# Performance work log

Hardware: AMD Instinct MI355X
Metric: run time of the kernel (lower is better)

Reference implementation:

```python
import jax, jax.numpy as jnp
import numpy as np
import math

B, CIN, COUT, K, SD, H, W = 16, 512, 512, 3, 512, 32, 32


def setup_inputs() -> dict:
    key = jax.random.key(0)
    ks = jax.random.split(key, 7)
    return {
        "x": jax.random.normal(ks[0], (B, CIN, H, W), jnp.float32),
        "style": jax.random.normal(ks[1], (B, SD), jnp.float32),
        "noise": jax.random.normal(ks[2], (B, 1, H, W), jnp.float32),
        "weight": jax.random.normal(ks[3], (COUT, CIN, K, K), jnp.float32),
        "mod_w": jax.random.normal(ks[4], (CIN, SD), jnp.float32),
        "mod_b": jnp.ones((CIN,), jnp.float32),
        "noise_weight": jax.random.normal(ks[5], (1,), jnp.float32) * 0.1,
        "act_bias": jax.random.normal(ks[6], (COUT,), jnp.float32) * 0.1,
    }


def reference(x, style, noise, weight, mod_w, mod_b, noise_weight, act_bias):
    conv_scale = 1.0 / math.sqrt(CIN * K * K)  # equalized-lr scale of ModulatedConv2d
    mod_scale = 1.0 / math.sqrt(SD)            # EqualLinear scale (lr_mul=1)

    # style modulation: EqualLinear(style_dim -> in_channel), bias init 1
    s = style @ (mod_w.T * mod_scale) + mod_b              # [B, CIN]

    # per-sample modulated weights [B, COUT, CIN, K, K]
    w = conv_scale * weight[None] * s[:, None, :, None, None]

    # demodulation
    demod = jax.lax.rsqrt(jnp.sum(w * w, axis=(2, 3, 4)) + 1e-8)  # [B, COUT]
    w = w * demod[:, :, None, None, None]

    # grouped (per-sample) conv: vmap a single-sample conv over the batch
    pad = K // 2

    def conv1(xi, wi):
        return jax.lax.conv_general_dilated(
            xi[None], wi, window_strides=(1, 1),
            padding=[(pad, pad), (pad, pad)],
            dimension_numbers=("NCHW", "OIHW", "NCHW"))[0]

    out = jax.vmap(conv1)(x, w)  # [B, COUT, H, W]

    # NoiseInjection: out + weight * noise (scalar learned weight)
    out = out + noise_weight[0] * noise

    # FusedLeakyReLU: leaky_relu(out + bias, 0.2) * sqrt(2)
    out = jax.nn.leaky_relu(out + act_bias[None, :, None, None], 0.2) * math.sqrt(2.0)
    return out
```

## Files before the change

### kernel.cpp

```cpp
#include <hip/hip_runtime.h>
#include <cstdint>
#include <cstddef>

typedef unsigned short u16;
typedef __attribute__((ext_vector_type(8))) short short8;
typedef __attribute__((ext_vector_type(4))) float f32x4;

#define CIN   512
#define COUT  512
#define BATCH 16
#define HWSZ  1024
#define PADW  34

static constexpr float MOD_SCALE  = 0.044194173824159216f;
static constexpr float CONV_SCALE = 0.014731391274719739f;

#define WS_S    0
#define WS_DSC  (32*1024)
#define WS_WSQ  (64*1024)
#define WS_WBT  (64*1024 + 1024*1024)
#define WS_XSP  (WS_WBT + 9*512*512*2)

__device__ __forceinline__ u16 f2bf(float f) {
  union { float f; uint32_t u; } v; v.f = f;
  uint32_t r = v.u + 0x7fffu + ((v.u >> 16) & 1u);
  return (u16)(r >> 16);
}

__device__ __forceinline__ void gload16(const void* g, void* l) {
  __builtin_amdgcn_global_load_lds(
      (const __attribute__((address_space(1))) void*)g,
      (__attribute__((address_space(3))) void*)l, 16, 0, 0);
}

__global__ void k_style(const float* __restrict__ style, const float* __restrict__ mod_w,
                        const float* __restrict__ mod_b, float* __restrict__ s_out) {
  int gid  = blockIdx.x * blockDim.x + threadIdx.x;
  int w    = gid >> 6, lane = gid & 63;
  int b    = w >> 9, i = w & 511;
  const float4* st = (const float4*)(style + (size_t)b * 512);
  const float4* mw = (const float4*)(mod_w + (size_t)i * 512);
  float4 a0 = st[lane * 2], a1 = st[lane * 2 + 1];
  float4 w0 = mw[lane * 2], w1 = mw[lane * 2 + 1];
  float acc = a0.x*w0.x + a0.y*w0.y + a0.z*w0.z + a0.w*w0.w
            + a1.x*w1.x + a1.y*w1.y + a1.z*w1.z + a1.w*w1.w;
  #pragma unroll
  for (int off = 32; off; off >>= 1) acc += __shfl_xor(acc, off);
  if (lane == 0) s_out[w] = acc * MOD_SCALE + mod_b[i];
}

__global__ void k_wprep(const float* __restrict__ w, float* __restrict__ wsq,
                        u16* __restrict__ wbt) {
  int idx = blockIdx.x * 256 + threadIdx.x;
  const float* p = w + (size_t)idx * 9;
  float a = 0.f;
  #pragma unroll
  for (int kxy = 0; kxy < 9; ++kxy) {
    float v = p[kxy];
    a += v * v;
    wbt[(size_t)kxy * 262144 + idx] = f2bf(v);
  }
  wsq[idx] = a;
}

__global__ void k_dscale(const float* __restrict__ wsq, const float* __restrict__ s,
                         float* __restrict__ dsc) {
  int gid  = blockIdx.x * blockDim.x + threadIdx.x;
  int w    = gid >> 6, lane = gid & 63;
  int b    = w >> 9, o = w & 511;
  const float4* q4 = (const float4*)(wsq + (size_t)o * 512);
  const float4* s4 = (const float4*)(s   + (size_t)b * 512);
  float4 q0 = q4[lane * 2], q1 = q4[lane * 2 + 1];
  float4 t0 = s4[lane * 2], t1 = s4[lane * 2 + 1];
  float acc = q0.x*t0.x*t0.x + q0.y*t0.y*t0.y + q0.z*t0.z*t0.z + q0.w*t0.w*t0.w
            + q1.x*t1.x*t1.x + q1.y*t1.y*t1.y + q1.z*t1.z*t1.z + q1.w*t1.w*t1.w;
  #pragma unroll
  for (int off = 32; off; off >>= 1) acc += __shfl_xor(acc, off);
  if (lane == 0)
    dsc[w] = CONV_SCALE * rsqrtf(acc * CONV_SCALE * CONV_SCALE + 1e-8f);
}

__global__ void k_xs(const float* __restrict__ x, const float* __restrict__ s,
                     u16* __restrict__ xsp) {
  __shared__ float tile[64][33];
  int icb = blockIdx.x, y = blockIdx.y, b = blockIdx.z;
  int t = threadIdx.x;
  int i0 = icb * 64;
  int c  = t & 31;
  int r0 = t >> 5;
  #pragma unroll
  for (int it = 0; it < 8; ++it) {
    int row = r0 + it * 8;
    float sv = s[b * 512 + i0 + row];
    tile[row][c] = x[((size_t)(b * 512 + i0 + row)) * 1024 + y * 32 + c] * sv;
  }
  __syncthreads();
  int il = t & 63;
  int x0 = t >> 6;
  #pragma unroll
  for (int it = 0; it < 8; ++it) {
    int xc = x0 + it * 4;
    xsp[((size_t)((b * PADW + y + 1) * PADW) + (xc + 1)) * 512 + i0 + il] = f2bf(tile[il][xc]);
  }
}

__global__ __launch_bounds__(256) void k_conv(
    const u16* __restrict__ wbt, const u16* __restrict__ xsp,
    const float* __restrict__ dsc, const float* __restrict__ noise,
    const float* __restrict__ nw, const float* __restrict__ abias,
    float* __restrict__ out)
{
  __shared__ u16 Ald[128 * 64];
  __shared__ u16 Bld[128 * 64];

  const int tid  = threadIdx.x;
  const int wave = tid >> 6, lane = tid & 63;
  const int o0 = blockIdx.x * 128;
  const int m0 = blockIdx.y * 128;
  const int b  = m0 >> 10;

  const u16* gA[4]; const u16* gB[4]; u16* lA[4]; u16* lB[4];
  const int cc = (((lane & 7) ^ (lane >> 3)) * 8);
  #pragma unroll
  for (int q = 0; q < 4; ++q) {
    int r  = wave * 32 + q * 8 + (lane >> 3);
    gA[q] = wbt + (size_t)(o0 + r) * 512 + cc;
    int mg = m0 + r;
    int yy = (mg >> 5) & 31, xx = mg & 31;
    gB[q] = xsp + ((size_t)(b * PADW + yy) * PADW + xx) * 512 + cc;
    lA[q] = &Ald[(wave * 32 + q * 8) * 64];
    lB[q] = &Bld[(wave * 32 + q * 8) * 64];
  }

  f32x4 acc[4][4];
  #pragma unroll
  for (int i = 0; i < 4; ++i)
    #pragma unroll
    for (int j = 0; j < 4; ++j) acc[i][j] = (f32x4){0.f, 0.f, 0.f, 0.f};

  const int wo = (wave >> 1) * 64;
  const int wm = (wave & 1) * 64;
  const int lrow = lane & 15;
  const int lk   = (lane >> 4) * 8;
  const int rsw  = (lrow & 7) << 3;

  for (int ks = 0; ks < 72; ++ks) {
    int kxy = ks >> 3;
    int ib  = (ks & 7) << 6;
    int ky  = kxy / 3, kx = kxy - ky * 3;
    int offA = kxy * 262144 + ib;
    int offB = ((ky * PADW + kx) << 9) + ib;

    __syncthreads();
    #pragma unroll
    for (int q = 0; q < 4; ++q) gload16(gA[q] + offA, lA[q]);
    #pragma unroll
    for (int q = 0; q < 4; ++q) gload16(gB[q] + offB, lB[q]);
    asm volatile("s_waitcnt vmcnt(0)" ::: "memory");
    __syncthreads();

    #pragma unroll
    for (int kh = 0; kh < 2; ++kh) {
      int kos = (kh * 32 + lk) ^ rsw;
      short8 av[4], bv[4];
      #pragma unroll
      for (int mi = 0; mi < 4; ++mi)
        av[mi] = *(const short8*)&Ald[(wo + mi * 16 + lrow) * 64 + kos];
      #pragma unroll
      for (int ni = 0; ni < 4; ++ni)
        bv[ni] = *(const short8*)&Bld[(wm + ni * 16 + lrow) * 64 + kos];
      #pragma unroll
      for (int mi = 0; mi < 4; ++mi)
        #pragma unroll
        for (int ni = 0; ni < 4; ++ni)
          acc[mi][ni] = __builtin_amdgcn_mfma_f32_16x16x32_bf16(
              av[mi], bv[ni], acc[mi][ni], 0, 0, 0);
    }
  }

  const float nwv = nw[0];
  const int mrow = (lane >> 4) << 2;
  #pragma unroll
  for (int mi = 0; mi < 4; ++mi) {
    #pragma unroll
    for (int ni = 0; ni < 4; ++ni) {
      int mg = m0 + wm + ni * 16 + lrow;
      int hw = mg & 1023;
      float nz = nwv * noise[b * 1024 + hw];
      #pragma unroll
      for (int r = 0; r < 4; ++r) {
        int og = o0 + wo + mi * 16 + mrow + r;
        float v = acc[mi][ni][r] * dsc[b * 512 + og] + nz + abias[og];
        v = (v > 0.f ? v : 0.2f * v) * 1.4142135623730951f;
        out[(size_t)(b * 512 + og) * 1024 + hw] = v;
      }
    }
  }
}

extern "C" void kernel_launch(void* const* d_in, const int* in_sizes, int n_in,
                              void* d_out, int out_size, void* d_ws, size_t ws_size,
                              hipStream_t stream) {
  const float* x      = (const float*)d_in[0];
  const float* style  = (const float*)d_in[1];
  const float* noise  = (const float*)d_in[2];
  const float* weight = (const float*)d_in[3];
  const float* mod_w  = (const float*)d_in[4];
  const float* mod_b  = (const float*)d_in[5];
  const float* nw     = (const float*)d_in[6];
  const float* abias  = (const float*)d_in[7];
  float* out = (float*)d_out;

  char* ws = (char*)d_ws;
  float* s_buf = (float*)(ws + WS_S);
  float* dsc   = (float*)(ws + WS_DSC);
  float* wsq   = (float*)(ws + WS_WSQ);
  u16*   wbt   = (u16*)(ws + WS_WBT);
  u16*   xsp   = (u16*)(ws + WS_XSP);

  hipMemsetAsync(xsp, 0, (size_t)BATCH * PADW * PADW * 512 * 2, stream);

  k_style <<<2048, 256, 0, stream>>>(style, mod_w, mod_b, s_buf);
  k_wprep <<<1024, 256, 0, stream>>>(weight, wsq, wbt);
  k_dscale<<<2048, 256, 0, stream>>>(wsq, s_buf, dsc);
  k_xs    <<<dim3(8, 32, 16), 256, 0, stream>>>(x, s_buf, xsp);
  k_conv  <<<dim3(4, 128), 256, 0, stream>>>(wbt, xsp, dsc, noise, nw, abias, out);
}
```

Before: 126.6 us.

## Triple-buffer conv GEMM loads with larger 256x128 tiles and block swizzle

Rewrites the main loop of the implicit-GEMM conv as a three-stage LDS ring. Asynchronous global-to-LDS loads for later K-steps are issued before computing the current one, and partial vmcnt waits replace the full drain before each barrier. Blocks grow to 512 threads, each computing a 256x128 output tile, and a linear grid with a swizzled block index replaces the 2D grid. This hides global load latency behind MFMA work and lets the larger tile reuse each loaded activation more. The cost is about 144KB of LDS per block, which limits each CU to one resident block, and fewer blocks overall.

```diff
diff --git a/kernel.cpp b/kernel.cpp
--- a/kernel.cpp
+++ b/kernel.cpp
@@ -104,32 +104,40 @@
   }
 }
 
-__global__ __launch_bounds__(256) void k_conv(
+__global__ __launch_bounds__(512, 2) void k_conv(
     const u16* __restrict__ wbt, const u16* __restrict__ xsp,
     const float* __restrict__ dsc, const float* __restrict__ noise,
     const float* __restrict__ nw, const float* __restrict__ abias,
     float* __restrict__ out)
 {
-  __shared__ u16 Ald[128 * 64];
-  __shared__ u16 Bld[128 * 64];
+  __shared__ u16 Ald[3 * 16384];
+  __shared__ u16 Bld[3 * 8192];
 
   const int tid  = threadIdx.x;
   const int wave = tid >> 6, lane = tid & 63;
-  const int o0 = blockIdx.x * 128;
-  const int m0 = blockIdx.y * 128;
+
+  const int bid = blockIdx.x;
+  const int swz = (bid & 7) * 32 + (bid >> 3);
+  const int o0 = (swz >> 7) << 8;
+  const int m0 = (swz & 127) << 7;
   const int b  = m0 >> 10;
 
-  const u16* gA[4]; const u16* gB[4]; u16* lA[4]; u16* lB[4];
   const int cc = (((lane & 7) ^ (lane >> 3)) * 8);
+  const u16* gA[4]; int lAo[4];
   #pragma unroll
   for (int q = 0; q < 4; ++q) {
-    int r  = wave * 32 + q * 8 + (lane >> 3);
+    int r = wave * 32 + q * 8 + (lane >> 3);
     gA[q] = wbt + (size_t)(o0 + r) * 512 + cc;
+    lAo[q] = (wave * 32 + q * 8) * 64;
+  }
+  const u16* gB[2]; int lBo[2];
+  #pragma unroll
+  for (int q = 0; q < 2; ++q) {
+    int r = wave * 16 + q * 8 + (lane >> 3);
     int mg = m0 + r;
     int yy = (mg >> 5) & 31, xx = mg & 31;
     gB[q] = xsp + ((size_t)(b * PADW + yy) * PADW + xx) * 512 + cc;
-    lA[q] = &Ald[(wave * 32 + q * 8) * 64];
-    lB[q] = &Bld[(wave * 32 + q * 8) * 64];
+    lBo[q] = (wave * 16 + q * 8) * 64;
   }
 
   f32x4 acc[4][4];
@@ -144,31 +152,28 @@
   const int lk   = (lane >> 4) * 8;
   const int rsw  = (lrow & 7) << 3;
 
-  for (int ks = 0; ks < 72; ++ks) {
-    int kxy = ks >> 3;
-    int ib  = (ks & 7) << 6;
-    int ky  = kxy / 3, kx = kxy - ky * 3;
+  auto stage = [&](int ks, int sa, int sb) {
+    int kxy = ks >> 3, ib = (ks & 7) << 6;
+    int ky = kxy / 3, kx = kxy - ky * 3;
     int offA = kxy * 262144 + ib;
     int offB = ((ky * PADW + kx) << 9) + ib;
-
-    __syncthreads();
-    #pragma unroll
-    for (int q = 0; q < 4; ++q) gload16(gA[q] + offA, lA[q]);
-    #pragma unroll
-    for (int q = 0; q < 4; ++q) gload16(gB[q] + offB, lB[q]);
-    asm volatile("s_waitcnt vmcnt(0)" ::: "memory");
-    __syncthreads();
-
+    #pragma unroll
+    for (int q = 0; q < 4; ++q) gload16(gA[q] + offA, &Ald[sa + lAo[q]]);
+    #pragma unroll
+    for (int q = 0; q < 2; ++q) gload16(gB[q] + offB, &Bld[sb + lBo[q]]);
+  };
+
+  auto compute = [&](int ca, int cb) {
     #pragma unroll
     for (int kh = 0; kh < 2; ++kh) {
       int kos = (kh * 32 + lk) ^ rsw;
       short8 av[4], bv[4];
       #pragma unroll
       for (int mi = 0; mi < 4; ++mi)
-        av[mi] = *(const short8*)&Ald[(wo + mi * 16 + lrow) * 64 + kos];
+        av[mi] = *(const short8*)&Ald[ca + (wo + mi * 16 + lrow) * 64 + kos];
       #pragma unroll
       for (int ni = 0; ni < 4; ++ni)
-        bv[ni] = *(const short8*)&Bld[(wm + ni * 16 + lrow) * 64 + kos];
+        bv[ni] = *(const short8*)&Bld[cb + (wm + ni * 16 + lrow) * 64 + kos];
       #pragma unroll
       for (int mi = 0; mi < 4; ++mi)
         #pragma unroll
@@ -176,6 +181,26 @@
           acc[mi][ni] = __builtin_amdgcn_mfma_f32_16x16x32_bf16(
               av[mi], bv[ni], acc[mi][ni], 0, 0, 0);
     }
+  };
+
+  stage(0, 0, 0);
+  stage(1, 16384, 8192);
+
+  for (int t = 0; t < 24; ++t) {
+    int k0 = t * 3;
+    asm volatile("s_waitcnt vmcnt(6)" ::: "memory");
+    __builtin_amdgcn_s_barrier();
+    if (k0 + 2 < 72) stage(k0 + 2, 32768, 16384);
+    compute(0, 0);
+    asm volatile("s_waitcnt vmcnt(6)" ::: "memory");
+    __builtin_amdgcn_s_barrier();
+    if (k0 + 3 < 72) stage(k0 + 3, 0, 0);
+    compute(16384, 8192);
+    if (k0 + 2 == 71) { asm volatile("s_waitcnt vmcnt(0)" ::: "memory"); }
+    else              { asm volatile("s_waitcnt vmcnt(6)" ::: "memory"); }
+    __builtin_amdgcn_s_barrier();
+    if (k0 + 4 < 72) stage(k0 + 4, 16384, 8192);
+    compute(32768, 16384);
   }
 
   const float nwv = nw[0];
@@ -224,5 +249,5 @@
   k_wprep <<<1024, 256, 0, stream>>>(weight, wsq, wbt);
   k_dscale<<<2048, 256, 0, stream>>>(wsq, s_buf, dsc);
   k_xs    <<<dim3(8, 32, 16), 256, 0, stream>>>(x, s_buf, xsp);
-  k_conv  <<<dim3(4, 128), 256, 0, stream>>>(wbt, xsp, dsc, noise, nw, abias, out);
-}
+  k_conv  <<<256, 512, 0, stream>>>(wbt, xsp, dsc, noise, nw, abias, out);
+}
```

Result: faster. 114.7 us (-9.4%).
